# Optimization experiments

Hardware: AMD Instinct MI355X
Metric: run time of the kernel (lower is better)

Reference implementation:

```python
import jax, jax.numpy as jnp
import numpy as np

N_NODE = 50000
N_MOL = 1024
C_DIM = 128
M_DIM = 128
P_DIM = 64
RADIUS = 2
NEG_INF = -1e9


def _leaky(x):
    return jnp.where(x > 0, x, 0.01 * x)


def setup_inputs() -> dict:
    key = jax.random.key(0)
    ks = jax.random.split(key, 16)
    node_features = jax.random.normal(ks[0], (N_NODE, C_DIM), dtype=jnp.float32)
    pos_features = jax.random.normal(ks[1], (N_NODE, P_DIM), dtype=jnp.float32)
    # each node assigned to one molecule -> dense bipartite assignment matrix
    assign = np.arange(N_NODE) % N_MOL
    mat = np.zeros((N_MOL, N_NODE), dtype=np.float32)
    mat[assign, np.arange(N_NODE)] = 1.0
    mask = np.where(mat > 0, 0.0, NEG_INF).astype(np.float32)
    s = 0.05
    params = dict(
        map_W=jax.random.normal(ks[2], (M_DIM, C_DIM), dtype=jnp.float32) * s,
        map_b=jnp.zeros((M_DIM,), dtype=jnp.float32),
        attend_W=jax.random.normal(ks[3], (C_DIM, C_DIM + P_DIM), dtype=jnp.float32) * s,
        attend_b=jnp.zeros((C_DIM,), dtype=jnp.float32),
        align_W=jax.random.normal(ks[4], (1, M_DIM + C_DIM + P_DIM), dtype=jnp.float32) * s,
        align_b=jnp.zeros((1,), dtype=jnp.float32),
        gru_Wih=jax.random.normal(ks[5], (3 * M_DIM, C_DIM), dtype=jnp.float32) * s,
        gru_Whh=jax.random.normal(ks[6], (3 * M_DIM, M_DIM), dtype=jnp.float32) * s,
        gru_bih=jnp.zeros((3 * M_DIM,), dtype=jnp.float32),
        gru_bhh=jnp.zeros((3 * M_DIM,), dtype=jnp.float32),
    )
    return dict(node_features=node_features, pos_features=pos_features,
                mol_node_matrix=jnp.asarray(mat), mol_node_mask=jnp.asarray(mask),
                **params)


def _gru_cell(x, h, Wih, Whh, bih, bhh):
    gi = x @ Wih.T + bih          # [M, 3*m_dim]
    gh = h @ Whh.T + bhh
    ir, iz, inn = jnp.split(gi, 3, axis=-1)
    hr, hz, hn = jnp.split(gh, 3, axis=-1)
    r = jax.nn.sigmoid(ir + hr)
    z = jax.nn.sigmoid(iz + hz)
    n = jnp.tanh(inn + r * hn)
    return (1.0 - z) * n + z * h


def reference(node_features, pos_features, mol_node_matrix, mol_node_mask,
              map_W, map_b, attend_W, attend_b, align_W, align_b,
              gru_Wih, gru_Whh, gru_bih, gru_bhh):
    # mol_features: [M, m_dim]
    mol_features = mol_node_matrix @ _leaky(node_features @ map_W.T + map_b)
    np_cat = jnp.concatenate([node_features, pos_features], axis=-1)  # [N, c+p]
    for _ in range(RADIUS):
        h = np_cat @ attend_W.T + attend_b                            # [N, c_dim] (dropout p=0)
        node_mol = mol_node_matrix.T @ mol_features                   # [N, m_dim]
        a = _leaky(jnp.concatenate([node_mol, pos_features, node_features], -1)
                   @ align_W.T + align_b)                             # [N, 1]
        # mol_node_matrix @ diag(a) == column scaling (avoids O(N^2) diag)
        logits = mol_node_matrix * a[:, 0][None, :] + mol_node_mask   # [M, N]
        w = jax.nn.softmax(logits, axis=1)
        context = jax.nn.elu(w @ h)                                   # [M, c_dim]
        mol_features = jax.nn.relu(
            _gru_cell(context, mol_features, gru_Wih, gru_Whh, gru_bih, gru_bhh))
    return mol_features
```

## Files before the change

### kernel.cpp

```cpp
#include <hip/hip_runtime.h>
#include <hip/hip_bf16.h>
#include <math.h>

#define N_NODE 50000
#define N_MOL  1024
#define C_DIM  128
#define P_DIM  64
#define M_DIM  128
#define NM_REM 848
#define NVBLK  196

typedef __attribute__((ext_vector_type(8))) short bf16x8;
typedef __attribute__((ext_vector_type(4))) float f32x4;

static __device__ __forceinline__ short f2bf(float x) {
    __hip_bfloat16 h = __float2bfloat16(x);
    return *reinterpret_cast<short*>(&h);
}
static __device__ __forceinline__ float bfs2f(short s) {
    unsigned int u = ((unsigned int)(unsigned short)s) << 16;
    float f;
    __builtin_memcpy(&f, &u, 4);
    return f;
}
static __device__ __forceinline__ int off_of(int m) {
    return (m < NM_REM) ? 49 * m : NM_REM + 48 * m;
}

__global__ __launch_bounds__(256) void k_prep_guess(const float* __restrict__ mat,
                                                    const float* __restrict__ map_W,
                                                    const float* __restrict__ att_W,
                                                    const float* __restrict__ Wih,
                                                    const float* __restrict__ Whh,
                                                    const float* __restrict__ alignW,
                                                    short* __restrict__ Bbf,
                                                    short* __restrict__ Wihb,
                                                    short* __restrict__ Whhb,
                                                    int* __restrict__ list,
                                                    int* __restrict__ offsets,
                                                    int* __restrict__ flags) {
    const int NB = 272 * 192;
    const int NW = 384 * 128;
    int idx = blockIdx.x * 256 + threadIdx.x;
    if (idx < NB) {
        int r = idx / 192, k = idx - r * 192;
        float v = 0.f;
        if (r < 128) { if (k < 128) v = map_W[r * 128 + k]; }
        else if (r < 256) v = att_W[(size_t)(r - 128) * 192 + k];
        else if (r == 256) v = (k < 128) ? alignW[192 + k] : alignW[k];
        Bbf[idx] = f2bf(v);
    } else if (idx < NB + NW) {
        int j = idx - NB;
        Wihb[j] = f2bf(Wih[j]);
    } else if (idx < NB + 2 * NW) {
        int j = idx - NB - NW;
        Whhb[j] = f2bf(Whh[j]);
    }
    if (idx <= N_MOL) offsets[idx] = off_of(idx);
    if (idx < N_NODE) {
        int m = idx & (N_MOL - 1);
        list[off_of(m) + (idx >> 10)] = idx;
    }
    if (blockIdx.x < NVBLK) {
        __shared__ int s_bad;
        if (threadIdx.x == 0) s_bad = 0;
        __syncthreads();
        if (idx < N_NODE) {
            int m = idx & (N_MOL - 1);
            if (!(mat[(size_t)m * N_NODE + idx] > 0.5f)) atomicOr(&s_bad, 1);
        }
        __syncthreads();
        if (threadIdx.x == 0) flags[blockIdx.x] = s_bad;
    }
}

__global__ __launch_bounds__(1024) void k_fallback(const float4* __restrict__ mat4,
                                                   const int* __restrict__ flags,
                                                   int* __restrict__ assign,
                                                   int* __restrict__ offsets,
                                                   int* __restrict__ list) {
    __shared__ int s_any;
    __shared__ int s_scan[N_MOL];
    __shared__ int s_tile[4096];
    int t = threadIdx.x;
    if (t == 0) s_any = 0;
    __syncthreads();
    if (t < NVBLK && flags[t]) atomicOr(&s_any, 1);
    __syncthreads();
    if (s_any == 0) return;

    const int total4 = (N_MOL * N_NODE) / 4;
    for (int j = t; j < total4; j += 1024) {
        float4 v = mat4[j];
        float f[4] = {v.x, v.y, v.z, v.w};
#pragma unroll
        for (int c = 0; c < 4; ++c) {
            if (f[c] > 0.5f) {
                int idx = j * 4 + c;
                int m = idx / N_NODE;
                assign[idx - m * N_NODE] = m;
            }
        }
    }
    __syncthreads();
    s_scan[t] = 0;
    __syncthreads();
    for (int i = t; i < N_NODE; i += 1024) atomicAdd(&s_scan[assign[i]], 1);
    __syncthreads();
    for (int d = 1; d < N_MOL; d <<= 1) {
        int v = (t >= d) ? s_scan[t - d] : 0;
        __syncthreads();
        s_scan[t] += v;
        __syncthreads();
    }
    offsets[t + 1] = s_scan[t];
    if (t == 0) offsets[0] = 0;
    int base_off = (t == 0) ? 0 : s_scan[t - 1];
    __syncthreads();
    int cur = 0;
    for (int tb = 0; tb < N_NODE; tb += 4096) {
        for (int q = t; q < 4096; q += 1024)
            s_tile[q] = (tb + q < N_NODE) ? assign[tb + q] : -1;
        __syncthreads();
        int lim = (N_NODE - tb < 4096) ? (N_NODE - tb) : 4096;
        for (int q = 0; q < lim; ++q)
            if (s_tile[q] == t) list[base_off + (cur++)] = tb + q;
        __syncthreads();
    }
}

__global__ __launch_bounds__(256) void k_gemm_fused(const float* __restrict__ node,
                                                    const float* __restrict__ pos,
                                                    const int* __restrict__ list,
                                                    const short* __restrict__ Bbf,
                                                    const float* __restrict__ map_b,
                                                    const float* __restrict__ att_b,
                                                    __hip_bfloat16* __restrict__ mapped,
                                                    __hip_bfloat16* __restrict__ hbuf,
                                                    float* __restrict__ sbase) {
    __shared__ short smem[64 * 264];
    __shared__ int s_list[64];
    int t = threadIdx.x;
    int n0 = blockIdx.x * 64;

    if (t < 64) {
        int pr = n0 + t;
        s_list[t] = (pr < N_NODE) ? list[pr] : 0;
    }
    __syncthreads();

    for (int idx = t; idx < 64 * 48; idx += 256) {
        int row = idx / 48;
        int c4 = idx - row * 48;
        float4 v = make_float4(0.f, 0.f, 0.f, 0.f);
        if (n0 + row < N_NODE) {
            int id = s_list[row];
            if (c4 < 32) v = *(const float4*)&node[(size_t)id * C_DIM + c4 * 4];
            else         v = *(const float4*)&pos[(size_t)id * P_DIM + (c4 - 32) * 4];
        }
        ushort4 u;
        u.x = (unsigned short)f2bf(v.x);
        u.y = (unsigned short)f2bf(v.y);
        u.z = (unsigned short)f2bf(v.z);
        u.w = (unsigned short)f2bf(v.w);
        *(ushort4*)&smem[row * 264 + c4 * 4] = u;
    }
    __syncthreads();

    int wid = t >> 6, lane = t & 63;
    int wr = wid >> 1, wc = wid & 1;
    int lrow = lane & 15, lk = (lane >> 4) * 8;

    bf16x8 a[2][6];
#pragma unroll
    for (int mt = 0; mt < 2; ++mt)
#pragma unroll
        for (int k = 0; k < 6; ++k)
            a[mt][k] = *(const bf16x8*)&smem[(wr * 32 + mt * 16 + lrow) * 264 + k * 32 + lk];

    f32x4 acc[2][9] = {};
#pragma unroll
    for (int ct = 0; ct < 9; ++ct) {
        if (ct == 8 && wc == 0) break;
        int c0 = wc * 128 + ct * 16;
        bf16x8 b[6];
#pragma unroll
        for (int k = 0; k < 6; ++k)
            b[k] = *(const bf16x8*)&Bbf[(size_t)(c0 + lrow) * 192 + k * 32 + lk];
#pragma unroll
        for (int mt = 0; mt < 2; ++mt)
#pragma unroll
            for (int k = 0; k < 6; ++k)
                acc[mt][ct] = __builtin_amdgcn_mfma_f32_16x16x32_bf16(
                    a[mt][k], b[k], acc[mt][ct], 0, 0, 0);
    }

    __syncthreads();

#pragma unroll
    for (int ct = 0; ct < 8; ++ct) {
        int c = wc * 128 + ct * 16 + lrow;
        float bias = (c < 128) ? map_b[c] : att_b[c - 128];
#pragma unroll
        for (int mt = 0; mt < 2; ++mt) {
#pragma unroll
            for (int r = 0; r < 4; ++r) {
                int row = wr * 32 + mt * 16 + (lane >> 4) * 4 + r;
                float v = acc[mt][ct][r] + bias;
                if (c < 128) v = (v > 0.f) ? v : 0.01f * v;
                smem[row * 264 + c] = f2bf(v);
            }
        }
    }
    if (wc == 1 && lrow == 0) {
#pragma unroll
        for (int mt = 0; mt < 2; ++mt)
#pragma unroll
            for (int r = 0; r < 4; ++r) {
                int pr = n0 + wr * 32 + mt * 16 + (lane >> 4) * 4 + r;
                if (pr < N_NODE) sbase[pr] = acc[mt][8][r];
            }
    }
    __syncthreads();

    short* mp = (short*)mapped;
    short* hp = (short*)hbuf;
    for (int v = t; v < 64 * 16; v += 256) {
        int row = v >> 4, ch = v & 15;
        int pr = n0 + row;
        if (pr < N_NODE)
            *(bf16x8*)&mp[(size_t)pr * 128 + ch * 8] =
                *(const bf16x8*)&smem[row * 264 + ch * 8];
    }
    for (int v = t; v < 64 * 16; v += 256) {
        int row = v >> 4, ch = v & 15;
        int pr = n0 + row;
        if (pr < N_NODE)
            *(bf16x8*)&hp[(size_t)pr * 128 + ch * 8] =
                *(const bf16x8*)&smem[row * 264 + 128 + ch * 8];
    }
}

__global__ __launch_bounds__(256) void k_molrad(const __hip_bfloat16* __restrict__ mapped,
                                                const __hip_bfloat16* __restrict__ hbuf,
                                                const float* __restrict__ sbase,
                                                const float* __restrict__ alignW,
                                                const float* __restrict__ alignb,
                                                const short* __restrict__ Wihb,
                                                const short* __restrict__ Whhb,
                                                const float* __restrict__ bih,
                                                const float* __restrict__ bhh,
                                                const int* __restrict__ offsets,
                                                float* __restrict__ mol) {
    __shared__ short s_actx[16][136];
    __shared__ short s_amol[16][136];
    __shared__ float s_molf[4][128];
    int t = threadIdx.x;
    int w = t >> 6, lane = t & 63;
    int m0 = blockIdx.x * 4;
    int mymol = m0 + w;

    for (int i = t; i < 12 * 128; i += 256) {
        int r = 4 + (i >> 7), c = i & 127;
        s_actx[r][c] = 0;
        s_amol[r][c] = 0;
    }

    int off = offsets[mymol];
    int cnt = offsets[mymol + 1] - off;
    int Q = cnt * 16;

    const short* mbase = (const short*)mapped + (size_t)off * 128;
    float acc8[8] = {};
    for (int q = lane; q < Q; q += 64) {
        bf16x8 v = *(const bf16x8*)&mbase[q * 8];
#pragma unroll
        for (int jj = 0; jj < 8; ++jj) acc8[jj] += bfs2f(v[jj]);
    }
#pragma unroll
    for (int jj = 0; jj < 8; ++jj) {
        acc8[jj] += __shfl_xor(acc8[jj], 16);
        acc8[jj] += __shfl_xor(acc8[jj], 32);
    }
    if (lane < 16) {
#pragma unroll
        for (int jj = 0; jj < 8; ++jj) {
            int c = lane * 8 + jj;
            s_molf[w][c] = acc8[jj];
            s_amol[w][c] = f2bf(acc8[jj]);
        }
    }
    float aw0 = alignW[lane], aw1 = alignW[64 + lane];
    float ab = alignb[0];
    int lrow = lane & 15, lk = (lane >> 4) * 8;
    __syncthreads();

    for (int it = 0; it < 2; ++it) {
        float v = s_molf[w][lane] * aw0 + s_molf[w][64 + lane] * aw1;
#pragma unroll
        for (int d = 32; d > 0; d >>= 1) v += __shfl_xor(v, d);
        float dm = v + ab;

        float x = -1e30f;
        if (lane < cnt) {
            x = sbase[off + lane] + dm;
            x = (x > 0.f) ? x : 0.01f * x;
        }
        float mx = x;
#pragma unroll
        for (int d = 32; d > 0; d >>= 1) mx = fmaxf(mx, __shfl_xor(mx, d));
        float e = (lane < cnt) ? __expf(x - mx) : 0.f;
        float sm = e;
#pragma unroll
        for (int d = 32; d > 0; d >>= 1) sm += __shfl_xor(sm, d);
        float myw = e / sm;

        const short* hb = (const short*)hbuf + (size_t)off * 128;
        float c8[8] = {};
        for (int q = lane; q < Q; q += 64) {
            bf16x8 vv = *(const bf16x8*)&hb[q * 8];
            float wgt = __shfl(myw, q >> 4);
#pragma unroll
            for (int jj = 0; jj < 8; ++jj) c8[jj] += wgt * bfs2f(vv[jj]);
        }
#pragma unroll
        for (int jj = 0; jj < 8; ++jj) {
            c8[jj] += __shfl_xor(c8[jj], 16);
            c8[jj] += __shfl_xor(c8[jj], 32);
        }
        if (lane < 16) {
#pragma unroll
            for (int jj = 0; jj < 8; ++jj) {
                float cv = c8[jj];
                cv = (cv > 0.f) ? cv : (__expf(cv) - 1.f);
                s_actx[w][lane * 8 + jj] = f2bf(cv);
            }
        }
        __syncthreads();

        bf16x8 a_c[4], a_m[4];
#pragma unroll
        for (int k = 0; k < 4; ++k) {
            a_c[k] = *(const bf16x8*)&s_actx[lrow][k * 32 + lk];
            a_m[k] = *(const bf16x8*)&s_amol[lrow][k * 32 + lk];
        }
        f32x4 ai[6], ah[6];
#pragma unroll
        for (int j = 0; j < 6; ++j) { ai[j] = (f32x4){}; ah[j] = (f32x4){}; }
#pragma unroll
        for (int j = 0; j < 6; ++j) {
            int c0 = w * 32 + (j & 1) * 16 + (j >> 1) * 128;
#pragma unroll
            for (int k = 0; k < 4; ++k) {
                bf16x8 bi = *(const bf16x8*)&Wihb[(size_t)(c0 + lrow) * 128 + k * 32 + lk];
                ai[j] = __builtin_amdgcn_mfma_f32_16x16x32_bf16(a_c[k], bi, ai[j], 0, 0, 0);
                bf16x8 bh = *(const bf16x8*)&Whhb[(size_t)(c0 + lrow) * 128 + k * 32 + lk];
                ah[j] = __builtin_amdgcn_mfma_f32_16x16x32_bf16(a_m[k], bh, ah[j], 0, 0, 0);
            }
        }
        __syncthreads();

        if (lane < 16) {
#pragma unroll
            for (int j2 = 0; j2 < 2; ++j2) {
                int chan = w * 32 + j2 * 16 + lane;
                float br = bih[chan], bz = bih[128 + chan], bn = bih[256 + chan];
                float cr = bhh[chan], cz = bhh[128 + chan], cn = bhh[256 + chan];
#pragma unroll
                for (int r = 0; r < 4; ++r) {
                    float gir = ai[j2][r] + br;
                    float giz = ai[2 + j2][r] + bz;
                    float gin = ai[4 + j2][r] + bn;
                    float ghr = ah[j2][r] + cr;
                    float ghz = ah[2 + j2][r] + cz;
                    float ghn = ah[4 + j2][r] + cn;
                    float molc = s_molf[r][chan];
                    float rr = 1.f / (1.f + __expf(-(gir + ghr)));
                    float zz = 1.f / (1.f + __expf(-(giz + ghz)));
                    float nn = tanhf(gin + rr * ghn);
                    float o = fmaxf((1.f - zz) * nn + zz * molc, 0.f);
                    s_molf[r][chan] = o;
                    s_amol[r][chan] = f2bf(o);
                }
            }
        }
        __syncthreads();
    }

#pragma unroll
    for (int j = 0; j < 2; ++j) {
        int item = t + j * 256;
        int mm = item >> 7, c = item & 127;
        mol[(size_t)(m0 + mm) * 128 + c] = s_molf[mm][c];
    }
}

extern "C" void kernel_launch(void* const* d_in, const int* in_sizes, int n_in,
                              void* d_out, int out_size, void* d_ws, size_t ws_size,
                              hipStream_t stream) {
    const float* node   = (const float*)d_in[0];
    const float* pos    = (const float*)d_in[1];
    const float* mat    = (const float*)d_in[2];
    const float* map_W  = (const float*)d_in[4];
    const float* map_b  = (const float*)d_in[5];
    const float* att_W  = (const float*)d_in[6];
    const float* att_b  = (const float*)d_in[7];
    const float* alignW = (const float*)d_in[8];
    const float* alignb = (const float*)d_in[9];
    const float* gWih   = (const float*)d_in[10];
    const float* gWhh   = (const float*)d_in[11];
    const float* gbih   = (const float*)d_in[12];
    const float* gbhh   = (const float*)d_in[13];
    float* mol = (float*)d_out;

    size_t o = 0;
    auto alloc = [&](size_t bytes) { size_t r = o; o += (bytes + 255) & ~(size_t)255; return r; };
    char* ws = (char*)d_ws;
    int*   flags   = (int*)(ws + alloc((size_t)NVBLK * 4));
    int*   assign  = (int*)(ws + alloc((size_t)N_NODE * 4));
    int*   offsets = (int*)(ws + alloc((size_t)(N_MOL + 1) * 4));
    int*   list    = (int*)(ws + alloc((size_t)N_NODE * 4));
    short* Bbf     = (short*)(ws + alloc((size_t)272 * 192 * 2));
    short* Wihb    = (short*)(ws + alloc((size_t)384 * 128 * 2));
    short* Whhb    = (short*)(ws + alloc((size_t)384 * 128 * 2));
    __hip_bfloat16* mapped = (__hip_bfloat16*)(ws + alloc((size_t)N_NODE * 128 * 2));
    __hip_bfloat16* hbuf   = (__hip_bfloat16*)(ws + alloc((size_t)N_NODE * 128 * 2));
    float* sbase   = (float*)(ws + alloc((size_t)N_NODE * 4));

    int prep_items = 272 * 192 + 2 * 384 * 128;
    k_prep_guess<<<(prep_items + 255) / 256, 256, 0, stream>>>(
        mat, map_W, att_W, gWih, gWhh, alignW, Bbf, Wihb, Whhb, list, offsets, flags);
    k_fallback<<<1, 1024, 0, stream>>>((const float4*)mat, flags,
                                       assign, offsets, list);
    k_gemm_fused<<<(N_NODE + 63) / 64, 256, 0, stream>>>(node, pos, list, Bbf,
                                                         map_b, att_b,
                                                         mapped, hbuf, sbase);
    k_molrad<<<N_MOL / 4, 256, 0, stream>>>(mapped, hbuf, sbase, alignW, alignb,
                                            Wihb, Whhb, gbih, gbhh, offsets, mol);
}
```

Measured before the change: 82.59 us.

## Fuse per-molecule mapped-feature reduction into GEMM epilogue and cache h in LDS

The GEMM kernel now reduces the mapped node features per molecule inside its epilogue and writes at most two partial sums per molecule (one for a molecule that starts in the block, one for a molecule continuing from the previous block) into a small buffer. This removes the full N×128 bf16 mapped buffer write and its re-read in the molecule kernel. The molecule kernel also stages each molecule's h rows in shared memory on the first radius pass so the second pass reads LDS instead of global memory. The cost is a larger LDS footprint per block (64 KB), which can reduce occupancy. The partial-slot scheme also relies on a molecule spanning at most two 64-node blocks.

```diff
diff --git a/kernel.cpp b/kernel.cpp
--- a/kernel.cpp
+++ b/kernel.cpp
@@ -132,20 +132,37 @@
 __global__ __launch_bounds__(256) void k_gemm_fused(const float* __restrict__ node,
                                                     const float* __restrict__ pos,
                                                     const int* __restrict__ list,
+                                                    const int* __restrict__ offsets,
                                                     const short* __restrict__ Bbf,
                                                     const float* __restrict__ map_b,
                                                     const float* __restrict__ att_b,
-                                                    __hip_bfloat16* __restrict__ mapped,
                                                     __hip_bfloat16* __restrict__ hbuf,
-                                                    float* __restrict__ sbase) {
+                                                    float* __restrict__ sbase,
+                                                    float* __restrict__ molpart) {
     __shared__ short smem[64 * 264];
     __shared__ int s_list[64];
+    __shared__ int s_mid[64];
     int t = threadIdx.x;
     int n0 = blockIdx.x * 64;
 
     if (t < 64) {
         int pr = n0 + t;
-        s_list[t] = (pr < N_NODE) ? list[pr] : 0;
+        int mid = -1;
+        s_list[t] = 0;
+        if (pr < N_NODE) {
+            s_list[t] = list[pr];
+            int mg = (pr < 49 * NM_REM) ? pr / 49 : (pr - NM_REM) / 48;
+            if (offsets[mg] <= pr && pr < offsets[mg + 1]) mid = mg;
+            else {
+                int lo = 0, hi = N_MOL - 1;
+                while (lo < hi) {
+                    int mm = (lo + hi + 1) >> 1;
+                    if (offsets[mm] <= pr) lo = mm; else hi = mm - 1;
+                }
+                mid = lo;
+            }
+        }
+        s_mid[t] = mid;
     }
     __syncthreads();
 
@@ -223,15 +240,7 @@
     }
     __syncthreads();
 
-    short* mp = (short*)mapped;
     short* hp = (short*)hbuf;
-    for (int v = t; v < 64 * 16; v += 256) {
-        int row = v >> 4, ch = v & 15;
-        int pr = n0 + row;
-        if (pr < N_NODE)
-            *(bf16x8*)&mp[(size_t)pr * 128 + ch * 8] =
-                *(const bf16x8*)&smem[row * 264 + ch * 8];
-    }
     for (int v = t; v < 64 * 16; v += 256) {
         int row = v >> 4, ch = v & 15;
         int pr = n0 + row;
@@ -239,11 +248,38 @@
             *(bf16x8*)&hp[(size_t)pr * 128 + ch * 8] =
                 *(const bf16x8*)&smem[row * 264 + 128 + ch * 8];
     }
-}
-
-__global__ __launch_bounds__(256) void k_molrad(const __hip_bfloat16* __restrict__ mapped,
-                                                const __hip_bfloat16* __restrict__ hbuf,
+
+    if (t < 128) {
+        int col = t;
+        float acc2 = 0.f;
+        int cur = s_mid[0];
+        for (int row = 0; row < 64; ++row) {
+            int m = s_mid[row];
+            if (m < 0) break;
+            if (m != cur) {
+                int offm = offsets[cur];
+                int slot = (offm >= n0) ? 0 : 1;
+                molpart[slot * (N_MOL * 128) + cur * 128 + col] = acc2;
+                if (slot == 0 && offsets[cur + 1] <= n0 + 64)
+                    molpart[N_MOL * 128 + cur * 128 + col] = 0.f;
+                acc2 = 0.f;
+                cur = m;
+            }
+            acc2 += bfs2f(smem[row * 264 + col]);
+        }
+        if (cur >= 0) {
+            int offm = offsets[cur];
+            int slot = (offm >= n0) ? 0 : 1;
+            molpart[slot * (N_MOL * 128) + cur * 128 + col] = acc2;
+            if (slot == 0 && offsets[cur + 1] <= n0 + 64)
+                molpart[N_MOL * 128 + cur * 128 + col] = 0.f;
+        }
+    }
+}
+
+__global__ __launch_bounds__(256) void k_molrad(const __hip_bfloat16* __restrict__ hbuf,
                                                 const float* __restrict__ sbase,
+                                                const float* __restrict__ molpart,
                                                 const float* __restrict__ alignW,
                                                 const float* __restrict__ alignb,
                                                 const short* __restrict__ Wihb,
@@ -255,6 +291,7 @@
     __shared__ short s_actx[16][136];
     __shared__ short s_amol[16][136];
     __shared__ float s_molf[4][128];
+    __shared__ short s_hc[4][64 * 128];
     int t = threadIdx.x;
     int w = t >> 6, lane = t & 63;
     int m0 = blockIdx.x * 4;
@@ -270,25 +307,15 @@
     int cnt = offsets[mymol + 1] - off;
     int Q = cnt * 16;
 
-    const short* mbase = (const short*)mapped + (size_t)off * 128;
-    float acc8[8] = {};
-    for (int q = lane; q < Q; q += 64) {
-        bf16x8 v = *(const bf16x8*)&mbase[q * 8];
-#pragma unroll
-        for (int jj = 0; jj < 8; ++jj) acc8[jj] += bfs2f(v[jj]);
-    }
-#pragma unroll
-    for (int jj = 0; jj < 8; ++jj) {
-        acc8[jj] += __shfl_xor(acc8[jj], 16);
-        acc8[jj] += __shfl_xor(acc8[jj], 32);
-    }
-    if (lane < 16) {
-#pragma unroll
-        for (int jj = 0; jj < 8; ++jj) {
-            int c = lane * 8 + jj;
-            s_molf[w][c] = acc8[jj];
-            s_amol[w][c] = f2bf(acc8[jj]);
-        }
+    {
+        float a0 = molpart[(size_t)mymol * 128 + lane]
+                 + molpart[(size_t)N_MOL * 128 + (size_t)mymol * 128 + lane];
+        float a1 = molpart[(size_t)mymol * 128 + 64 + lane]
+                 + molpart[(size_t)N_MOL * 128 + (size_t)mymol * 128 + 64 + lane];
+        s_molf[w][lane] = a0;
+        s_molf[w][64 + lane] = a1;
+        s_amol[w][lane] = f2bf(a0);
+        s_amol[w][64 + lane] = f2bf(a1);
     }
     float aw0 = alignW[lane], aw1 = alignW[64 + lane];
     float ab = alignb[0];
@@ -315,13 +342,23 @@
         for (int d = 32; d > 0; d >>= 1) sm += __shfl_xor(sm, d);
         float myw = e / sm;
 
-        const short* hb = (const short*)hbuf + (size_t)off * 128;
         float c8[8] = {};
-        for (int q = lane; q < Q; q += 64) {
-            bf16x8 vv = *(const bf16x8*)&hb[q * 8];
-            float wgt = __shfl(myw, q >> 4);
-#pragma unroll
-            for (int jj = 0; jj < 8; ++jj) c8[jj] += wgt * bfs2f(vv[jj]);
+        if (it == 0) {
+            const short* hb = (const short*)hbuf + (size_t)off * 128;
+            for (int q = lane; q < Q; q += 64) {
+                bf16x8 vv = *(const bf16x8*)&hb[q * 8];
+                *(bf16x8*)&s_hc[w][q * 8] = vv;
+                float wgt = __shfl(myw, q >> 4);
+#pragma unroll
+                for (int jj = 0; jj < 8; ++jj) c8[jj] += wgt * bfs2f(vv[jj]);
+            }
+        } else {
+            for (int q = lane; q < Q; q += 64) {
+                bf16x8 vv = *(const bf16x8*)&s_hc[w][q * 8];
+                float wgt = __shfl(myw, q >> 4);
+#pragma unroll
+                for (int jj = 0; jj < 8; ++jj) c8[jj] += wgt * bfs2f(vv[jj]);
+            }
         }
 #pragma unroll
         for (int jj = 0; jj < 8; ++jj) {
@@ -423,18 +460,18 @@
     short* Bbf     = (short*)(ws + alloc((size_t)272 * 192 * 2));
     short* Wihb    = (short*)(ws + alloc((size_t)384 * 128 * 2));
     short* Whhb    = (short*)(ws + alloc((size_t)384 * 128 * 2));
-    __hip_bfloat16* mapped = (__hip_bfloat16*)(ws + alloc((size_t)N_NODE * 128 * 2));
-    __hip_bfloat16* hbuf   = (__hip_bfloat16*)(ws + alloc((size_t)N_NODE * 128 * 2));
+    __hip_bfloat16* hbuf = (__hip_bfloat16*)(ws + alloc((size_t)N_NODE * 128 * 2));
     float* sbase   = (float*)(ws + alloc((size_t)N_NODE * 4));
+    float* molpart = (float*)(ws + alloc((size_t)2 * N_MOL * 128 * 4));
 
     int prep_items = 272 * 192 + 2 * 384 * 128;
     k_prep_guess<<<(prep_items + 255) / 256, 256, 0, stream>>>(
         mat, map_W, att_W, gWih, gWhh, alignW, Bbf, Wihb, Whhb, list, offsets, flags);
     k_fallback<<<1, 1024, 0, stream>>>((const float4*)mat, flags,
                                        assign, offsets, list);
-    k_gemm_fused<<<(N_NODE + 63) / 64, 256, 0, stream>>>(node, pos, list, Bbf,
+    k_gemm_fused<<<(N_NODE + 63) / 64, 256, 0, stream>>>(node, pos, list, offsets, Bbf,
                                                          map_b, att_b,
-                                                         mapped, hbuf, sbase);
-    k_molrad<<<N_MOL / 4, 256, 0, stream>>>(mapped, hbuf, sbase, alignW, alignb,
+                                                         hbuf, sbase, molpart);
+    k_molrad<<<N_MOL / 4, 256, 0, stream>>>(hbuf, sbase, molpart, alignW, alignb,
                                             Wihb, Whhb, gbih, gbhh, offsets, mol);
 }
```

New measurement: 83.06 us. About the same (+0.6%).
